# Performance work log

Hardware: AMD Instinct MI355X
Metric: run time of the kernel (lower is better)

## Reference

```python
import jax, jax.numpy as jnp
import numpy as np
from jax import lax

D = 1024
N_EXP = 8
DD = 4 * D
BS = 8192
TRAIN_CAP = 1.0
LN_EPS = 1e-5


def setup_inputs() -> dict:
    key = jax.random.key(0)
    ks = jax.random.split(key, 8)
    s = 0.02
    return {
        "x": jax.random.normal(ks[0], (BS, D), jnp.float32),
        "Wg": jax.random.normal(ks[1], (N_EXP, D), jnp.float32) * s,
        "cp_w1": jax.random.normal(ks[2], (D, D), jnp.float32) * s,
        "cp_b1": jnp.zeros((D,), jnp.float32),
        "cp_w2": jax.random.normal(ks[3], (N_EXP, D), jnp.float32) * s,
        "cp_b2": jnp.zeros((N_EXP,), jnp.float32),
        "ln_g": jnp.ones((D,), jnp.float32),
        "ln_b": jnp.zeros((D,), jnp.float32),
        "fc1s": jax.random.normal(ks[4], (N_EXP, DD, D), jnp.float32) * s,
        "b1s": jnp.zeros((N_EXP, DD), jnp.float32),
        "fc2s": jax.random.normal(ks[5], (N_EXP, D, DD), jnp.float32) * s,
        "b2s": jnp.zeros((N_EXP, D), jnp.float32),
    }


def reference(x, Wg, cp_w1, cp_b1, cp_w2, cp_b2, ln_g, ln_b, fc1s, b1s, fc2s, b2s):
    bs, d = x.shape
    n = Wg.shape[0]
    k = int(bs * TRAIN_CAP) // n  # tokens kept per expert

    # gate scores in (0,1): (tanh(x Wg^T)+1)/2   -> [bs, n]
    scores = (jnp.tanh(x @ Wg.T) + 1.0) * 0.5

    # per-expert descending sort of tokens by score
    order = jnp.argsort(-scores, axis=0)                      # [bs, n]
    sorted_w = jnp.take_along_axis(scores, order, axis=0)     # [bs, n]
    kept_w = sorted_w[:k]                                     # [k, n]
    kept_idx = order[:k]                                      # [k, n]

    # keep mask (labels for capacity predictor)
    keep_mask = jnp.zeros((bs, n), x.dtype).at[kept_idx, jnp.arange(n)[None, :]].set(1.0)

    # capacity predictor loss (BCE with logits, x detached)
    xd = lax.stop_gradient(x)
    h = jax.nn.gelu(xd @ cp_w1.T + cp_b1, approximate=True)
    logits = h @ cp_w2.T + cp_b2                              # [bs, n]
    cap_loss = jnp.mean(jnp.logaddexp(0.0, logits) - logits * keep_mask)

    # dispatch: gather selected tokens, row-major flatten of [k, n]
    idx = kept_idx.reshape(-1)                                # [k*n]
    y = x[idx]                                                # [k*n, d]

    # LayerNorm
    mu = y.mean(-1, keepdims=True)
    var = y.var(-1, keepdims=True)
    y = (y - mu) * lax.rsqrt(var + LN_EPS) * ln_g + ln_b

    # per-expert grouped GEMMs
    y3 = y.reshape(k, n, d)
    h1 = jnp.einsum('knd,nfd->knf', y3, fc1s) + b1s[None]     # [k, n, dd]
    h1 = jax.nn.gelu(h1, approximate=True)
    y2 = jnp.einsum('knf,ndf->knd', h1, fc2s) + b2s[None]     # [k, n, d]

    # weight by gate score and scatter-add back (residual)
    y2 = y2 * kept_w[..., None]
    out = x.at[idx].add(y2.reshape(k * n, d))
    return out, cap_loss
```

## Files before the change

### kernel.cpp

```cpp
#include <hip/hip_runtime.h>


#define BS_   8192
#define D_    1024
#define DD_   4096
#define NEXP  8
#define KCAP  1024

typedef unsigned int   uint32;
typedef unsigned short u16;
typedef __bf16 bf16x8  __attribute__((ext_vector_type(8)));
typedef float  f32x4   __attribute__((ext_vector_type(4)));
typedef u16    u16x8   __attribute__((ext_vector_type(8)));
typedef u16    u16x4   __attribute__((ext_vector_type(4)));

__device__ __forceinline__ u16 f2bf(float f){
  uint32 u = __float_as_uint(f);
  u = (u + 0x7fffu + ((u >> 16) & 1u)) >> 16;
  return (u16)u;
}
__device__ __forceinline__ float bf_lo(uint32 u){ return __uint_as_float(u << 16); }
__device__ __forceinline__ float bf_hi(uint32 u){ return __uint_as_float(u & 0xffff0000u); }

__device__ __forceinline__ float gelu_fast(float v){
  const float u2 = v * (1.5957691216057308f + 0.07135481282962162f * v * v);
  const float e  = __expf(u2);
  return v - v / (1.0f + e);
}
__device__ __forceinline__ void glds16(const u16* g, u16* l){
  __builtin_amdgcn_global_load_lds(
      (const __attribute__((address_space(1))) unsigned int*)g,
      (__attribute__((address_space(3))) unsigned int*)l, 16, 0, 0);
}

__global__ __launch_bounds__(256)
void pack_b_kernel(const float* __restrict__ in, u16* __restrict__ out,
                   int K, int kshift)
{
  const long long t = (long long)blockIdx.x * 256 + threadIdx.x;
  const int  lane  = (int)(t & 63);
  const long long brick = t >> 6;
  const long long n16 = brick >> kshift;
  const int  k32  = (int)(brick & ((1 << kshift) - 1));
  const float* src = in + (n16 * 16 + (lane & 15)) * (long long)K
                        + k32 * 32 + (lane >> 4) * 8;
  const float4 a = *(const float4*)src;
  const float4 b = *(const float4*)(src + 4);
  u16x8 o;
  o[0]=f2bf(a.x); o[1]=f2bf(a.y); o[2]=f2bf(a.z); o[3]=f2bf(a.w);
  o[4]=f2bf(b.x); o[5]=f2bf(b.y); o[6]=f2bf(b.z); o[7]=f2bf(b.w);
  *(u16x8*)(out + t * 8) = o;
}

__global__ __launch_bounds__(64)
void gating_kernel(const float* __restrict__ x, const float* __restrict__ Wg,
                   float* __restrict__ scores, uint32* __restrict__ keep_bits,
                   u16* __restrict__ xh)
{
  const int i    = blockIdx.x;
  const int lane = threadIdx.x;
  const float* xr = x + (size_t)i * D_ + lane * 16;
  const float4 x0 = *(const float4*)(xr +  0);
  const float4 x1 = *(const float4*)(xr +  4);
  const float4 x2 = *(const float4*)(xr +  8);
  const float4 x3 = *(const float4*)(xr + 12);
  u16x8 p0, p1;
  p0[0]=f2bf(x0.x); p0[1]=f2bf(x0.y); p0[2]=f2bf(x0.z); p0[3]=f2bf(x0.w);
  p0[4]=f2bf(x1.x); p0[5]=f2bf(x1.y); p0[6]=f2bf(x1.z); p0[7]=f2bf(x1.w);
  p1[0]=f2bf(x2.x); p1[1]=f2bf(x2.y); p1[2]=f2bf(x2.z); p1[3]=f2bf(x2.w);
  p1[4]=f2bf(x3.x); p1[5]=f2bf(x3.y); p1[6]=f2bf(x3.z); p1[7]=f2bf(x3.w);
  *(u16x8*)(xh + (size_t)i * D_ + lane * 16)     = p0;
  *(u16x8*)(xh + (size_t)i * D_ + lane * 16 + 8) = p1;

  float acc[NEXP];
  #pragma unroll
  for (int e = 0; e < NEXP; e++){
    const float* wr = Wg + e * D_ + lane * 16;
    const float4 w0 = *(const float4*)(wr +  0);
    const float4 w1 = *(const float4*)(wr +  4);
    const float4 w2 = *(const float4*)(wr +  8);
    const float4 w3 = *(const float4*)(wr + 12);
    float s = x0.x*w0.x + x0.y*w0.y + x0.z*w0.z + x0.w*w0.w;
    s += x1.x*w1.x + x1.y*w1.y + x1.z*w1.z + x1.w*w1.w;
    s += x2.x*w2.x + x2.y*w2.y + x2.z*w2.z + x2.w*w2.w;
    s += x3.x*w3.x + x3.y*w3.y + x3.z*w3.z + x3.w*w3.w;
    acc[e] = s;
  }
  #pragma unroll
  for (int e = 0; e < NEXP; e++){
    #pragma unroll
    for (int off = 32; off >= 1; off >>= 1) acc[e] += __shfl_xor(acc[e], off);
  }
  if (lane == 0){
    #pragma unroll
    for (int e = 0; e < NEXP; e++) scores[i * NEXP + e] = (tanhf(acc[e]) + 1.0f) * 0.5f;
    keep_bits[i] = 0u;
  }
}

__global__ __launch_bounds__(256)
void select_kernel(const float* __restrict__ scores, uint32* __restrict__ keep_bits,
                   int* __restrict__ counts, int* __restrict__ rowlist,
                   float* __restrict__ wlist, int* __restrict__ inv)
{
  __shared__ unsigned long long sk[2048];
  const int e = blockIdx.y;
  const int i = blockIdx.x * 256 + threadIdx.x;
  const float ms = scores[i * NEXP + e];
  const unsigned long long mk =
      ((unsigned long long)__float_as_uint(ms) << 32) | (uint32)(BS_ - 1 - i);
  int cnt = 0;
  for (int base = 0; base < BS_; base += 2048){
    #pragma unroll
    for (int u = 0; u < 8; u++){
      const int j = base + (int)threadIdx.x * 8 + u;
      const float sj = scores[j * NEXP + e];
      sk[threadIdx.x * 8 + u] =
          ((unsigned long long)__float_as_uint(sj) << 32) | (uint32)(BS_ - 1 - j);
    }
    __syncthreads();
    #pragma unroll 8
    for (int jj = 0; jj < 2048; jj++) cnt += (sk[jj] > mk) ? 1 : 0;
    __syncthreads();
  }
  if (cnt < KCAP){
    const int slot = atomicAdd(&counts[e], 1);
    rowlist[e * KCAP + slot] = i;
    wlist[e * KCAP + slot]   = ms;
    inv[i * NEXP + e]        = slot;
    atomicOr(&keep_bits[i], 1u << e);
  }
}

template<bool GELU_EP, bool OUT_BF16, int SPLIT>
__global__ __launch_bounds__(256)
void gemm_pk(const u16* __restrict__ A, const u16* __restrict__ Bp,
             const float* __restrict__ bias, void* __restrict__ Cv,
             float* __restrict__ P0, float* __restrict__ P1,
             int M, int N, int K,
             long long sA, long long sBp, long long sBias, long long sC)
{
  __shared__ u16 smA[128 * 32];
  const int zr   = blockIdx.z;
  const int z    = zr / SPLIT, ks = zr % SPLIT;
  const int kb0  = (K / SPLIT) * ks;
  const int kIt0 = kb0 >> 5, kIt1 = (kb0 + K / SPLIT) >> 5;
  const int m0   = blockIdx.y * 128;
  const int n0   = blockIdx.x * 128;
  const int tid  = threadIdx.x;
  const int lane = tid & 63, wv = tid >> 6;
  const int l15  = lane & 15, quad = lane >> 4;
  const int moff = (wv >> 1) * 64, noff = (wv & 1) * 64;

  const int srow = wv * 32 + (lane >> 2);
  const int skol = (lane & 3) * 8;
  const u16* Ag = A + (long long)z * sA + (long long)(m0 + srow) * K + skol;
  u16* lA = smA + wv * 1024;

  const int nk32 = K >> 5;
  const long long jstr = (long long)nk32 * 512;
  const u16* Bfrag = Bp + (long long)z * sBp
                   + ((long long)((n0 + noff) >> 4)) * jstr + (long long)lane * 8;

  f32x4 acc[4][4];
  #pragma unroll
  for (int i = 0; i < 4; i++)
    #pragma unroll
    for (int j = 0; j < 4; j++)
      acc[i][j] = (f32x4){0.f, 0.f, 0.f, 0.f};

  bf16x8 bF[4], bN[4];
  #pragma unroll
  for (int j = 0; j < 4; j++)
    bF[j] = *(const bf16x8*)(Bfrag + j * jstr + (long long)kIt0 * 512);

  for (int kk = kIt0; kk < kIt1; kk++){
    glds16(Ag + kk * 32,           lA);
    glds16(Ag + 16 * K + kk * 32,  lA + 512);
    __syncthreads();
    const bool more = (kk + 1 < kIt1);
    if (more){
      #pragma unroll
      for (int j = 0; j < 4; j++)
        bN[j] = *(const bf16x8*)(Bfrag + j * jstr + (long long)(kk + 1) * 512);
    }
    bf16x8 aF[4];
    #pragma unroll
    for (int i = 0; i < 4; i++)
      aF[i] = *(const bf16x8*)(smA + (moff + i * 16 + l15) * 32 + quad * 8);
    #pragma unroll
    for (int i = 0; i < 4; i++)
      #pragma unroll
      for (int j = 0; j < 4; j++)
        acc[i][j] = __builtin_amdgcn_mfma_f32_16x16x32_bf16(bF[j], aF[i], acc[i][j], 0, 0, 0);
    __syncthreads();
    if (more){
      #pragma unroll
      for (int j = 0; j < 4; j++) bF[j] = bN[j];
    }
  }

  if constexpr (SPLIT > 1){
    float* Pout = (ks == 0 ? P0 : P1) + (long long)z * sC;
    #pragma unroll
    for (int i = 0; i < 4; i++){
      const int gm = m0 + moff + i * 16 + l15;
      #pragma unroll
      for (int j = 0; j < 4; j++){
        const int gn = n0 + noff + j * 16 + quad * 4;
        *(float4*)(Pout + (long long)gm * N + gn) =
            make_float4(acc[i][j][0], acc[i][j][1], acc[i][j][2], acc[i][j][3]);
      }
    }
  } else {
    const float* biasp = bias + (long long)z * sBias;
    const long long cbase = (long long)z * sC;
    #pragma unroll
    for (int i = 0; i < 4; i++){
      const int gm = m0 + moff + i * 16 + l15;
      const long long rowb = cbase + (long long)gm * N;
      #pragma unroll
      for (int j = 0; j < 4; j++){
        const int gn = n0 + noff + j * 16 + quad * 4;
        const float4 bv = *(const float4*)(biasp + gn);
        float v0 = acc[i][j][0] + bv.x;
        float v1 = acc[i][j][1] + bv.y;
        float v2 = acc[i][j][2] + bv.z;
        float v3 = acc[i][j][3] + bv.w;
        if constexpr (GELU_EP){
          v0 = gelu_fast(v0); v1 = gelu_fast(v1);
          v2 = gelu_fast(v2); v3 = gelu_fast(v3);
        }
        if constexpr (OUT_BF16){
          u16x4 o; o[0]=f2bf(v0); o[1]=f2bf(v1); o[2]=f2bf(v2); o[3]=f2bf(v3);
          *(u16x4*)((u16*)Cv + rowb + gn) = o;
        } else {
          *(float4*)((float*)Cv + rowb + gn) = make_float4(v0, v1, v2, v3);
        }
      }
    }
  }
}

__global__ __launch_bounds__(256)
void loss_kernel(const u16* __restrict__ h, const float* __restrict__ cp_w2,
                 const float* __restrict__ cp_b2, const uint32* __restrict__ keep_bits,
                 float* __restrict__ loss)
{
  __shared__ float bl;
  if (threadIdx.x == 0) bl = 0.f;
  __syncthreads();
  const int wv = threadIdx.x >> 6, lane = threadIdx.x & 63;
  const int i  = blockIdx.x * 4 + wv;
  const u16* hr = h + (size_t)i * D_ + lane * 16;
  const uint4 ha = *(const uint4*)(hr);
  const uint4 hb = *(const uint4*)(hr + 8);
  float hx[16];
  hx[0]=bf_lo(ha.x); hx[1]=bf_hi(ha.x); hx[2]=bf_lo(ha.y); hx[3]=bf_hi(ha.y);
  hx[4]=bf_lo(ha.z); hx[5]=bf_hi(ha.z); hx[6]=bf_lo(ha.w); hx[7]=bf_hi(ha.w);
  hx[8]=bf_lo(hb.x); hx[9]=bf_hi(hb.x); hx[10]=bf_lo(hb.y); hx[11]=bf_hi(hb.y);
  hx[12]=bf_lo(hb.z); hx[13]=bf_hi(hb.z); hx[14]=bf_lo(hb.w); hx[15]=bf_hi(hb.w);
  float acc[NEXP];
  #pragma unroll
  for (int e = 0; e < NEXP; e++){
    const float* wr = cp_w2 + e * D_ + lane * 16;
    const float4 w0 = *(const float4*)(wr +  0);
    const float4 w1 = *(const float4*)(wr +  4);
    const float4 w2 = *(const float4*)(wr +  8);
    const float4 w3 = *(const float4*)(wr + 12);
    float s = hx[0]*w0.x + hx[1]*w0.y + hx[2]*w0.z + hx[3]*w0.w;
    s += hx[4]*w1.x + hx[5]*w1.y + hx[6]*w1.z + hx[7]*w1.w;
    s += hx[8]*w2.x + hx[9]*w2.y + hx[10]*w2.z + hx[11]*w2.w;
    s += hx[12]*w3.x + hx[13]*w3.y + hx[14]*w3.z + hx[15]*w3.w;
    acc[e] = s;
  }
  #pragma unroll
  for (int e = 0; e < NEXP; e++){
    #pragma unroll
    for (int off = 32; off >= 1; off >>= 1) acc[e] += __shfl_xor(acc[e], off);
  }
  if (lane == 0){
    const uint32 kb = keep_bits[i];
    float li = 0.f;
    #pragma unroll
    for (int e = 0; e < NEXP; e++){
      const float l  = acc[e] + cp_b2[e];
      const float sp = fmaxf(l, 0.f) + log1pf(expf(-fabsf(l)));
      li += sp - l * (float)((kb >> e) & 1u);
    }
    atomicAdd(&bl, li);
  }
  __syncthreads();
  if (threadIdx.x == 0) atomicAdd(loss, bl);
}

__global__ __launch_bounds__(256)
void ln_gather_kernel(const float* __restrict__ x, const int* __restrict__ rowlist,
                      const float* __restrict__ ln_g, const float* __restrict__ ln_b,
                      u16* __restrict__ Y)
{
  __shared__ float red[8];
  const int b   = blockIdx.x;
  const int row = rowlist[b];
  const int tid = threadIdx.x;
  const float4 v = *(const float4*)(x + (size_t)row * D_ + tid * 4);
  float s = v.x + v.y + v.z + v.w;
  float q = v.x*v.x + v.y*v.y + v.z*v.z + v.w*v.w;
  const int lane = tid & 63, wv = tid >> 6;
  #pragma unroll
  for (int off = 32; off >= 1; off >>= 1){ s += __shfl_xor(s, off); q += __shfl_xor(q, off); }
  if (lane == 0){ red[wv] = s; red[4 + wv] = q; }
  __syncthreads();
  s = red[0] + red[1] + red[2] + red[3];
  q = red[4] + red[5] + red[6] + red[7];
  const float mu  = s * (1.0f / D_);
  const float var = q * (1.0f / D_) - mu * mu;
  const float rs  = rsqrtf(var + 1e-5f);
  const float4 g  = *(const float4*)(ln_g + tid * 4);
  const float4 bb = *(const float4*)(ln_b + tid * 4);
  u16x4 o;
  o[0] = f2bf((v.x - mu) * rs * g.x + bb.x);
  o[1] = f2bf((v.y - mu) * rs * g.y + bb.y);
  o[2] = f2bf((v.z - mu) * rs * g.z + bb.z);
  o[3] = f2bf((v.w - mu) * rs * g.w + bb.w);
  *(u16x4*)(&Y[(size_t)b * D_ + tid * 4]) = o;
}

__global__ __launch_bounds__(256)
void combine_kernel(const float* __restrict__ x, const uint32* __restrict__ keep_bits,
                    const int* __restrict__ inv, const float* __restrict__ wlist,
                    const float* __restrict__ P0, const float* __restrict__ P1,
                    const float* __restrict__ b2s, float* __restrict__ out)
{
  const int i = blockIdx.x;
  const int c = threadIdx.x * 4;
  float4 v = *(const float4*)(x + (size_t)i * D_ + c);
  uint32 kb = keep_bits[i];
  while (kb){
    const int e = __ffs(kb) - 1;
    kb &= kb - 1;
    const int r = inv[i * NEXP + e];
    const float w = wlist[e * KCAP + r];
    const size_t ro = ((size_t)(e * KCAP + r)) * D_ + c;
    const float4 p0 = *(const float4*)(P0 + ro);
    const float4 p1 = *(const float4*)(P1 + ro);
    const float4 b2 = *(const float4*)(b2s + (size_t)e * D_ + c);
    v.x += w * (p0.x + p1.x + b2.x);
    v.y += w * (p0.y + p1.y + b2.y);
    v.z += w * (p0.z + p1.z + b2.z);
    v.w += w * (p0.w + p1.w + b2.w);
  }
  *(float4*)(out + (size_t)i * D_ + c) = v;
}

__global__ void finalize_loss_kernel(const float* __restrict__ loss, float* __restrict__ outp){
  outp[0] = loss[0] * (1.0f / (float)(BS_ * NEXP));
}

extern "C" void kernel_launch(void* const* d_in, const int* in_sizes, int n_in,
                              void* d_out, int out_size, void* d_ws, size_t ws_size,
                              hipStream_t stream)
{
  const float* x     = (const float*)d_in[0];
  const float* Wg    = (const float*)d_in[1];
  const float* cp_w1 = (const float*)d_in[2];
  const float* cp_b1 = (const float*)d_in[3];
  const float* cp_w2 = (const float*)d_in[4];
  const float* cp_b2 = (const float*)d_in[5];
  const float* ln_g  = (const float*)d_in[6];
  const float* ln_b  = (const float*)d_in[7];
  const float* fc1s  = (const float*)d_in[8];
  const float* b1s   = (const float*)d_in[9];
  const float* fc2s  = (const float*)d_in[10];
  const float* b2s   = (const float*)d_in[11];
  float* out = (float*)d_out;

  char* p = (char*)d_ws;
  auto take = [&](size_t bytes) -> char* {
    char* r = p; p += (bytes + 255) & ~(size_t)255; return r;
  };
  float*  scores    = (float*) take((size_t)BS_ * NEXP * 4);
  int*    counts    = (int*)   take(256);
  float*  loss      = (float*) take(256);
  int*    rowlist   = (int*)   take((size_t)BS_ * 4);
  float*  wlist     = (float*) take((size_t)BS_ * 4);
  uint32* keep_bits = (uint32*)take((size_t)BS_ * 4);
  int*    inv       = (int*)   take((size_t)BS_ * NEXP * 4);
  u16*    xh        = (u16*)   take((size_t)BS_ * D_ * 2);
  u16*    cpw1p     = (u16*)   take((size_t)D_ * D_ * 2);
  u16*    fc1p      = (u16*)   take((size_t)NEXP * DD_ * D_ * 2);
  u16*    fc2p      = (u16*)   take((size_t)NEXP * D_ * DD_ * 2);
  u16*    H1        = (u16*)   take((size_t)NEXP * KCAP * DD_ * 2);
  u16*    h_cp      = (u16*)   take((size_t)BS_ * D_ * 2);
  u16*    Y         = (u16*)   take((size_t)NEXP * KCAP * D_ * 2);
  float*  Pt0       = (float*)xh;
  float*  Pt1       = (float*)((char*)xh + ((size_t)32 << 20));

  hipMemsetAsync(counts, 0, 512, stream);

  pack_b_kernel<<<(D_ * D_ / 8) / 256, 256, 0, stream>>>(cp_w1, cpw1p, D_, 5);
  pack_b_kernel<<<(NEXP * DD_ * D_ / 8) / 256, 256, 0, stream>>>(fc1s, fc1p, D_, 5);
  pack_b_kernel<<<(NEXP * D_ * DD_ / 8) / 256, 256, 0, stream>>>(fc2s, fc2p, DD_, 7);

  gating_kernel<<<BS_, 64, 0, stream>>>(x, Wg, scores, keep_bits, xh);

  select_kernel<<<dim3(BS_ / 256, NEXP), 256, 0, stream>>>(
      scores, keep_bits, counts, rowlist, wlist, inv);

  gemm_pk<true, true, 1><<<dim3(D_ / 128, BS_ / 128, 1), 256, 0, stream>>>(
      xh, cpw1p, cp_b1, h_cp, nullptr, nullptr, BS_, D_, D_, 0, 0, 0, 0);

  loss_kernel<<<BS_ / 4, 256, 0, stream>>>(h_cp, cp_w2, cp_b2, keep_bits, loss);

  ln_gather_kernel<<<BS_, 256, 0, stream>>>(x, rowlist, ln_g, ln_b, Y);

  gemm_pk<true, true, 1><<<dim3(DD_ / 128, KCAP / 128, NEXP), 256, 0, stream>>>(
      Y, fc1p, b1s, H1, nullptr, nullptr, KCAP, DD_, D_,
      (long long)KCAP * D_, (long long)DD_ * D_, DD_, (long long)KCAP * DD_);

  gemm_pk<false, false, 2><<<dim3(D_ / 128, KCAP / 128, NEXP * 2), 256, 0, stream>>>(
      H1, fc2p, nullptr, nullptr, Pt0, Pt1, KCAP, D_, DD_,
      (long long)KCAP * DD_, (long long)D_ * DD_, 0, (long long)KCAP * D_);

  combine_kernel<<<BS_, 256, 0, stream>>>(x, keep_bits, inv, wlist, Pt0, Pt1, b2s, out);

  finalize_loss_kernel<<<1, 1, 0, stream>>>(loss, out + (size_t)BS_ * D_);
}
```

Measured before the change: 851.4 us.

## Pack A operands in MFMA fragment layout and stage both A and B through LDS

The producers of GEMM A operands (gating bf16 cast, LN gather, and the fc1 epilogue) now write in the same 16x32 fragment-packed layout already used for the weights. The GEMM loads both A and B tiles into shared memory with direct global-to-LDS copies and reads fragments contiguously, replacing the register-prefetched B path. This targets scattered row-strided A loads and bank-unfriendly LDS reads. In exchange, the B register double-buffering is gone, so global-load latency for B is no longer overlapped with compute, and LDS traffic doubles.

```diff
diff --git a/kernel.cpp b/kernel.cpp
--- a/kernel.cpp
+++ b/kernel.cpp
@@ -69,8 +69,10 @@
   p0[4]=f2bf(x1.x); p0[5]=f2bf(x1.y); p0[6]=f2bf(x1.z); p0[7]=f2bf(x1.w);
   p1[0]=f2bf(x2.x); p1[1]=f2bf(x2.y); p1[2]=f2bf(x2.z); p1[3]=f2bf(x2.w);
   p1[4]=f2bf(x3.x); p1[5]=f2bf(x3.y); p1[6]=f2bf(x3.z); p1[7]=f2bf(x3.w);
-  *(u16x8*)(xh + (size_t)i * D_ + lane * 16)     = p0;
-  *(u16x8*)(xh + (size_t)i * D_ + lane * 16 + 8) = p1;
+  u16* dst = xh + ((size_t)(i >> 4) * 32 + (lane >> 1)) * 512
+                + (lane & 1) * 256 + (i & 15) * 8;
+  *(u16x8*)dst         = p0;
+  *(u16x8*)(dst + 128) = p1;
 
   float acc[NEXP];
   #pragma unroll
@@ -132,19 +134,20 @@
   }
 }
 
-template<bool GELU_EP, bool OUT_BF16, int SPLIT>
-__global__ __launch_bounds__(256)
-void gemm_pk(const u16* __restrict__ A, const u16* __restrict__ Bp,
+template<int MODE, int SPLIT>
+__global__ __launch_bounds__(256)
+void gemm_br(const u16* __restrict__ A, const u16* __restrict__ B,
              const float* __restrict__ bias, void* __restrict__ Cv,
              float* __restrict__ P0, float* __restrict__ P1,
              int M, int N, int K,
-             long long sA, long long sBp, long long sBias, long long sC)
-{
-  __shared__ u16 smA[128 * 32];
+             long long sA, long long sB, long long sBias, long long sC)
+{
+  __shared__ u16 smA[8 * 512];
+  __shared__ u16 smB[8 * 512];
   const int zr   = blockIdx.z;
   const int z    = zr / SPLIT, ks = zr % SPLIT;
-  const int kb0  = (K / SPLIT) * ks;
-  const int kIt0 = kb0 >> 5, kIt1 = (kb0 + K / SPLIT) >> 5;
+  const int nk   = K >> 5;
+  const int kIt0 = (nk / SPLIT) * ks, kIt1 = kIt0 + nk / SPLIT;
   const int m0   = blockIdx.y * 128;
   const int n0   = blockIdx.x * 128;
   const int tid  = threadIdx.x;
@@ -152,15 +155,9 @@
   const int l15  = lane & 15, quad = lane >> 4;
   const int moff = (wv >> 1) * 64, noff = (wv & 1) * 64;
 
-  const int srow = wv * 32 + (lane >> 2);
-  const int skol = (lane & 3) * 8;
-  const u16* Ag = A + (long long)z * sA + (long long)(m0 + srow) * K + skol;
-  u16* lA = smA + wv * 1024;
-
-  const int nk32 = K >> 5;
-  const long long jstr = (long long)nk32 * 512;
-  const u16* Bfrag = Bp + (long long)z * sBp
-                   + ((long long)((n0 + noff) >> 4)) * jstr + (long long)lane * 8;
+  const u16* Apk = A + (long long)z * sA + (long long)((m0 >> 4) + wv * 2) * nk * 512 + lane * 8;
+  const u16* Bpk = B + (long long)z * sB + (long long)((n0 >> 4) + wv * 2) * nk * 512 + lane * 8;
+  const long long nstr = (long long)nk * 512;
 
   f32x4 acc[4][4];
   #pragma unroll
@@ -169,38 +166,28 @@
     for (int j = 0; j < 4; j++)
       acc[i][j] = (f32x4){0.f, 0.f, 0.f, 0.f};
 
-  bf16x8 bF[4], bN[4];
-  #pragma unroll
-  for (int j = 0; j < 4; j++)
-    bF[j] = *(const bf16x8*)(Bfrag + j * jstr + (long long)kIt0 * 512);
-
   for (int kk = kIt0; kk < kIt1; kk++){
-    glds16(Ag + kk * 32,           lA);
-    glds16(Ag + 16 * K + kk * 32,  lA + 512);
+    glds16(Apk +         (long long)kk * 512, smA + (wv * 2    ) * 512);
+    glds16(Apk + nstr +  (long long)kk * 512, smA + (wv * 2 + 1) * 512);
+    glds16(Bpk +         (long long)kk * 512, smB + (wv * 2    ) * 512);
+    glds16(Bpk + nstr +  (long long)kk * 512, smB + (wv * 2 + 1) * 512);
     __syncthreads();
-    const bool more = (kk + 1 < kIt1);
-    if (more){
-      #pragma unroll
-      for (int j = 0; j < 4; j++)
-        bN[j] = *(const bf16x8*)(Bfrag + j * jstr + (long long)(kk + 1) * 512);
-    }
-    bf16x8 aF[4];
+    bf16x8 aF[4], bF[4];
     #pragma unroll
     for (int i = 0; i < 4; i++)
-      aF[i] = *(const bf16x8*)(smA + (moff + i * 16 + l15) * 32 + quad * 8);
+      aF[i] = *(const bf16x8*)(smA + ((wv >> 1) * 4 + i) * 512 + lane * 8);
+    #pragma unroll
+    for (int j = 0; j < 4; j++)
+      bF[j] = *(const bf16x8*)(smB + ((wv & 1) * 4 + j) * 512 + lane * 8);
     #pragma unroll
     for (int i = 0; i < 4; i++)
       #pragma unroll
       for (int j = 0; j < 4; j++)
         acc[i][j] = __builtin_amdgcn_mfma_f32_16x16x32_bf16(bF[j], aF[i], acc[i][j], 0, 0, 0);
     __syncthreads();
-    if (more){
-      #pragma unroll
-      for (int j = 0; j < 4; j++) bF[j] = bN[j];
-    }
-  }
-
-  if constexpr (SPLIT > 1){
+  }
+
+  if constexpr (MODE == 2){
     float* Pout = (ks == 0 ? P0 : P1) + (long long)z * sC;
     #pragma unroll
     for (int i = 0; i < 4; i++){
@@ -215,27 +202,26 @@
   } else {
     const float* biasp = bias + (long long)z * sBias;
     const long long cbase = (long long)z * sC;
+    const int nkO = N >> 5;
     #pragma unroll
     for (int i = 0; i < 4; i++){
       const int gm = m0 + moff + i * 16 + l15;
-      const long long rowb = cbase + (long long)gm * N;
       #pragma unroll
       for (int j = 0; j < 4; j++){
         const int gn = n0 + noff + j * 16 + quad * 4;
         const float4 bv = *(const float4*)(biasp + gn);
-        float v0 = acc[i][j][0] + bv.x;
-        float v1 = acc[i][j][1] + bv.y;
-        float v2 = acc[i][j][2] + bv.z;
-        float v3 = acc[i][j][3] + bv.w;
-        if constexpr (GELU_EP){
-          v0 = gelu_fast(v0); v1 = gelu_fast(v1);
-          v2 = gelu_fast(v2); v3 = gelu_fast(v3);
-        }
-        if constexpr (OUT_BF16){
-          u16x4 o; o[0]=f2bf(v0); o[1]=f2bf(v1); o[2]=f2bf(v2); o[3]=f2bf(v3);
-          *(u16x4*)((u16*)Cv + rowb + gn) = o;
+        float v0 = gelu_fast(acc[i][j][0] + bv.x);
+        float v1 = gelu_fast(acc[i][j][1] + bv.y);
+        float v2 = gelu_fast(acc[i][j][2] + bv.z);
+        float v3 = gelu_fast(acc[i][j][3] + bv.w);
+        u16x4 o; o[0]=f2bf(v0); o[1]=f2bf(v1); o[2]=f2bf(v2); o[3]=f2bf(v3);
+        if constexpr (MODE == 0){
+          *(u16x4*)((u16*)Cv + cbase + (long long)gm * N + gn) = o;
         } else {
-          *(float4*)((float*)Cv + rowb + gn) = make_float4(v0, v1, v2, v3);
+          u16* dst = (u16*)Cv + cbase
+                   + ((long long)(gm >> 4) * nkO + (gn >> 5)) * 512
+                   + ((gn >> 3) & 3) * 128 + (gm & 15) * 8 + (gn & 7);
+          *(u16x4*)dst = o;
         }
       }
     }
@@ -300,9 +286,11 @@
                       u16* __restrict__ Y)
 {
   __shared__ float red[8];
-  const int b   = blockIdx.x;
-  const int row = rowlist[b];
-  const int tid = threadIdx.x;
+  const int b    = blockIdx.x;
+  const int e    = b >> 10;
+  const int slot = b & (KCAP - 1);
+  const int row  = rowlist[b];
+  const int tid  = threadIdx.x;
   const float4 v = *(const float4*)(x + (size_t)row * D_ + tid * 4);
   float s = v.x + v.y + v.z + v.w;
   float q = v.x*v.x + v.y*v.y + v.z*v.z + v.w*v.w;
@@ -323,7 +311,10 @@
   o[1] = f2bf((v.y - mu) * rs * g.y + bb.y);
   o[2] = f2bf((v.z - mu) * rs * g.z + bb.z);
   o[3] = f2bf((v.w - mu) * rs * g.w + bb.w);
-  *(u16x4*)(&Y[(size_t)b * D_ + tid * 4]) = o;
+  u16* dst = Y + (size_t)e * KCAP * D_
+           + ((size_t)(slot >> 4) * 32 + (tid >> 3)) * 512
+           + ((tid >> 1) & 3) * 128 + (slot & 15) * 8 + (tid & 1) * 4;
+  *(u16x4*)dst = o;
 }
 
 __global__ __launch_bounds__(256)
@@ -407,18 +398,18 @@
   select_kernel<<<dim3(BS_ / 256, NEXP), 256, 0, stream>>>(
       scores, keep_bits, counts, rowlist, wlist, inv);
 
-  gemm_pk<true, true, 1><<<dim3(D_ / 128, BS_ / 128, 1), 256, 0, stream>>>(
+  gemm_br<0, 1><<<dim3(D_ / 128, BS_ / 128, 1), 256, 0, stream>>>(
       xh, cpw1p, cp_b1, h_cp, nullptr, nullptr, BS_, D_, D_, 0, 0, 0, 0);
 
   loss_kernel<<<BS_ / 4, 256, 0, stream>>>(h_cp, cp_w2, cp_b2, keep_bits, loss);
 
   ln_gather_kernel<<<BS_, 256, 0, stream>>>(x, rowlist, ln_g, ln_b, Y);
 
-  gemm_pk<true, true, 1><<<dim3(DD_ / 128, KCAP / 128, NEXP), 256, 0, stream>>>(
+  gemm_br<1, 1><<<dim3(DD_ / 128, KCAP / 128, NEXP), 256, 0, stream>>>(
       Y, fc1p, b1s, H1, nullptr, nullptr, KCAP, DD_, D_,
       (long long)KCAP * D_, (long long)DD_ * D_, DD_, (long long)KCAP * DD_);
 
-  gemm_pk<false, false, 2><<<dim3(D_ / 128, KCAP / 128, NEXP * 2), 256, 0, stream>>>(
+  gemm_br<2, 2><<<dim3(D_ / 128, KCAP / 128, NEXP * 2), 256, 0, stream>>>(
       H1, fc2p, nullptr, nullptr, Pt0, Pt1, KCAP, D_, DD_,
       (long long)KCAP * DD_, (long long)D_ * DD_, 0, (long long)KCAP * D_);
 
```

After: 917.9 us. +7.8%, slower.
